# Optimization experiments

Hardware: AMD Instinct MI355X
Metric: run time of the kernel (lower is better)

## Reference

```python
import jax, jax.numpy as jnp
import numpy as np

B = 8388608
NUM_CLASSES = 3
ALPHA = 0.25
GAMMA = 2.0
CRIT_PENALTY = 50.0
PENALTY = np.array([[0.0, 2.0, 5.0], [8.0, 0.0, 3.0], [50.0, 20.0, 0.0]], dtype=np.float32)


def setup_inputs() -> dict:
    key = jax.random.key(0)
    k1, k2 = jax.random.split(key)
    outputs = jax.random.normal(k1, (B, NUM_CLASSES), dtype=jnp.float32)
    targets = jax.random.randint(k2, (B,), 0, NUM_CLASSES, dtype=jnp.int64)
    class_weights = jnp.array([1.0, 2.0, 5.0], dtype=jnp.float32)
    penalty_matrix = jnp.asarray(PENALTY)
    return {"outputs": outputs, "targets": targets,
            "class_weights": class_weights, "penalty_matrix": penalty_matrix}


def reference(outputs, targets, class_weights, penalty_matrix):
    # log-softmax once; per-sample CE
    log_p = jax.nn.log_softmax(outputs, axis=1)                     # [B, C]
    ce_raw = -jnp.take_along_axis(log_p, targets[:, None], axis=1)[:, 0]  # [B]

    # weighted CE with mean reduction (torch: sum(w_t * ce) / sum(w_t))
    w_t = class_weights[targets]                                    # [B]
    ce_loss = jnp.sum(w_t * ce_raw) / jnp.sum(w_t)

    # focal component
    pt = jnp.exp(-ce_raw)
    focal_loss = jnp.mean(ALPHA * (1.0 - pt) ** GAMMA * ce_raw)

    # safety penalty: vectorized gather penalty_matrix[true, pred]
    pred_classes = jnp.argmax(outputs, axis=1)                      # [B]
    safety_penalty = jnp.mean(penalty_matrix[targets, pred_classes])

    # critical-miss penalty (class 2)
    critical_mask = targets == 2
    n_crit = jnp.sum(critical_mask)
    misses = jnp.sum(critical_mask & (pred_classes != 2)).astype(jnp.float32)
    critical_penalty = jnp.where(
        n_crit > 0,
        misses / jnp.maximum(n_crit, 1).astype(jnp.float32) * CRIT_PENALTY,
        0.0,
    )

    total = ce_loss + 0.3 * focal_loss + 0.4 * safety_penalty + 0.6 * critical_penalty
    return total
```

## Files before the change

### kernel.cpp

```cpp
#include <hip/hip_runtime.h>


#define THREADS 256
#define SAMPLES 8
#define SPB (THREADS * SAMPLES)

__global__ __launch_bounds__(THREADS) void loss_main(
    const float* __restrict__ outp,
    const int*   __restrict__ tgt,
    const float* __restrict__ cw,
    const float* __restrict__ pen,
    float*       __restrict__ partial,
    int n, int nblocks)
{
    __shared__ float4 lut[9];
    const int tid = threadIdx.x;
    if (tid < 9) {
        int t = (tid >= 6) ? 2 : ((tid >= 3) ? 1 : 0);
        int p = tid - t * 3;
        float4 e;
        e.x = pen[tid];
        e.y = cw[t];
        e.z = (t == 1) ? 4096.f : ((t == 2) ? 1.f : 0.f);
        e.w = (t == 2 && p != 2) ? 1.f : 0.f;
        lut[tid] = e;
    }
    __syncthreads();

    float s_wce = 0.f, s_f = 0.f, s_s = 0.f, s_cnt = 0.f, s_miss = 0.f;

    const long long base = ((long long)blockIdx.x * THREADS + tid) * SAMPLES;

    if (base + SAMPLES - 1 < n) {
        const float4* o4 = (const float4*)(outp + base * 3);
        const int4*   t4 = (const int4*)(tgt + base);
        float xf[3 * SAMPLES];
        *(float4*)&xf[ 0] = o4[0]; *(float4*)&xf[ 4] = o4[1]; *(float4*)&xf[ 8] = o4[2];
        *(float4*)&xf[12] = o4[3]; *(float4*)&xf[16] = o4[4]; *(float4*)&xf[20] = o4[5];
        int ti[SAMPLES];
        *(int4*)&ti[0] = t4[0]; *(int4*)&ti[4] = t4[1];

#pragma unroll
        for (int k = 0; k < SAMPLES; ++k) {
            float x0 = xf[3*k+0], x1 = xf[3*k+1], x2 = xf[3*k+2];
            int t = ti[k];
            float e0 = __expf(x0);
            float e1 = __expf(x1);
            float e2 = __expf(x2);
            float s  = e0 + e1 + e2;
            bool  t0 = (t == 0), t1 = (t == 1);
            float xt = t0 ? x0 : (t1 ? x1 : x2);
            float et = t0 ? e0 : (t1 ? e1 : e2);
            float ce = __logf(s) - xt;
            float pt = __fdividef(et, s);
            bool  g10 = (x1 > x0);
            int   pred = g10 ? 1 : 0;
            float xp   = g10 ? x1 : x0;
            if (x2 > xp) pred = 2;

            float4 L = lut[t * 3 + pred];
            s_s   += L.x;
            s_wce += L.y * ce;
            float om = 1.f - pt;
            s_f   += om * om * ce;
            s_cnt += L.z;
            s_miss+= L.w;
        }
    } else {
        for (int k = 0; k < SAMPLES; ++k) {
            long long i = base + k;
            if (i >= n) break;
            float x0 = outp[i*3+0], x1 = outp[i*3+1], x2 = outp[i*3+2];
            int t = tgt[i];
            float e0 = __expf(x0), e1 = __expf(x1), e2 = __expf(x2);
            float s  = e0 + e1 + e2;
            bool  t0 = (t == 0), t1 = (t == 1);
            float xt = t0 ? x0 : (t1 ? x1 : x2);
            float et = t0 ? e0 : (t1 ? e1 : e2);
            float ce = __logf(s) - xt;
            float pt = __fdividef(et, s);
            bool  g10 = (x1 > x0);
            int   pred = g10 ? 1 : 0;
            float xp   = g10 ? x1 : x0;
            if (x2 > xp) pred = 2;
            float4 L = lut[t * 3 + pred];
            s_s   += L.x;
            s_wce += L.y * ce;
            float om = 1.f - pt;
            s_f   += om * om * ce;
            s_cnt += L.z;
            s_miss+= L.w;
        }
    }

#pragma unroll
    for (int off = 32; off > 0; off >>= 1) {
        s_wce  += __shfl_down(s_wce,  off);
        s_f    += __shfl_down(s_f,    off);
        s_s    += __shfl_down(s_s,    off);
        s_cnt  += __shfl_down(s_cnt,  off);
        s_miss += __shfl_down(s_miss, off);
    }

    __shared__ float fred[4][5];
    const int lane = tid & 63;
    const int wave = tid >> 6;
    if (lane == 0) {
        fred[wave][0] = s_wce; fred[wave][1] = s_f;  fred[wave][2] = s_s;
        fred[wave][3] = s_cnt; fred[wave][4] = s_miss;
    }
    __syncthreads();
    if (tid < 5) {
        float v = fred[0][tid] + fred[1][tid] + fred[2][tid] + fred[3][tid];
        partial[tid * nblocks + blockIdx.x] = v;
    }
}

__global__ __launch_bounds__(256) void loss_finalize(
    const float* __restrict__ partial,
    float* __restrict__ out, int nblocks, int n)
{
    double a_wce = 0, a_f = 0, a_s = 0, a_n1 = 0, a_n2 = 0, a_miss = 0;
    for (int i = threadIdx.x; i < nblocks; i += 256) {
        a_wce += (double)partial[0 * nblocks + i];
        a_f   += (double)partial[1 * nblocks + i];
        a_s   += (double)partial[2 * nblocks + i];
        float c  = partial[3 * nblocks + i];
        float n1 = floorf(c * (1.f / 4096.f));
        a_n1 += (double)n1;
        a_n2 += (double)(c - n1 * 4096.f);
        a_miss += (double)partial[4 * nblocks + i];
    }
    double acc[6] = {a_wce, a_f, a_s, a_n1, a_n2, a_miss};
#pragma unroll
    for (int off = 32; off > 0; off >>= 1) {
#pragma unroll
        for (int j = 0; j < 6; ++j)
            acc[j] += __shfl_down(acc[j], off);
    }
    __shared__ double dred[4][6];
    const int lane = threadIdx.x & 63;
    const int wave = threadIdx.x >> 6;
    if (lane == 0) {
#pragma unroll
        for (int j = 0; j < 6; ++j) dred[wave][j] = acc[j];
    }
    __syncthreads();
    if (threadIdx.x == 0) {
        double t[6];
#pragma unroll
        for (int j = 0; j < 6; ++j)
            t[j] = dred[0][j] + dred[1][j] + dred[2][j] + dred[3][j];
        double n1 = t[3], n2 = t[4];
        double s_w = (double)n + n1 + 4.0 * n2;
        double inv_b   = 1.0 / (double)n;
        double ce_loss = t[0] / s_w;
        double focal   = 0.25 * t[1] * inv_b;
        double safety  = t[2] * inv_b;
        double crit    = (n2 > 0.0) ? (t[5] / n2 * 50.0) : 0.0;
        out[0] = (float)(ce_loss + 0.3 * focal + 0.4 * safety + 0.6 * crit);
    }
}

extern "C" void kernel_launch(void* const* d_in, const int* in_sizes, int n_in,
                              void* d_out, int out_size, void* d_ws, size_t ws_size,
                              hipStream_t stream) {
    const float* outp = (const float*)d_in[0];
    const int*   tgt  = (const int*)d_in[1];
    const float* cw   = (const float*)d_in[2];
    const float* pen  = (const float*)d_in[3];
    float* out = (float*)d_out;
    const int n = in_sizes[1];

    const int nblocks = (n + SPB - 1) / SPB;
    float* partial = (float*)d_ws;

    loss_main<<<nblocks, THREADS, 0, stream>>>(outp, tgt, cw, pen, partial, n, nblocks);
    loss_finalize<<<1, 256, 0, stream>>>(partial, out, nblocks, n);
}
```

Measured before the change: 179.9 us.

## Switch to persistent grid-stride blocks with register double-buffered tile loads

Replaces the one-tile-per-block launch (4096 blocks) with a fixed grid of 1024 persistent blocks that loop over tiles of 4 samples per thread, prefetching the next tile into registers while the current one is computed. The packed class-1/class-2 count encoding is split into two separate accumulators, which simplifies the finalize step, and the finalize now reduces a fixed 1024 partials. This aims to hide memory latency and cut block launch and reduction overhead for a bandwidth-bound kernel. In exchange each thread issues smaller loads per iteration and the loop adds control overhead, and occupancy depends on 1024 blocks being enough to fill the GPU.

Result: slower. 184.2 us (+2.4%).

```diff
diff --git a/kernel.cpp b/kernel.cpp
--- a/kernel.cpp
+++ b/kernel.cpp
@@ -2,8 +2,23 @@
 
 
 #define THREADS 256
-#define SAMPLES 8
+#define SAMPLES 4
 #define SPB (THREADS * SAMPLES)
+#define NB 1024
+
+typedef float f32x4 __attribute__((ext_vector_type(4)));
+typedef int   i32x4 __attribute__((ext_vector_type(4)));
+
+struct TileRegs {
+    f32x4 o0, o1, o2;
+    i32x4 t0;
+};
+
+__device__ __forceinline__ void load_tile(TileRegs& r, const float* op, const int* tp) {
+    const f32x4* o4 = (const f32x4*)op;
+    r.o0 = o4[0]; r.o1 = o4[1]; r.o2 = o4[2];
+    r.t0 = *(const i32x4*)tp;
+}
 
 __global__ __launch_bounds__(THREADS) void loss_main(
     const float* __restrict__ outp,
@@ -11,7 +26,7 @@
     const float* __restrict__ cw,
     const float* __restrict__ pen,
     float*       __restrict__ partial,
-    int n, int nblocks)
+    int n)
 {
     __shared__ float4 lut[9];
     const int tid = threadIdx.x;
@@ -21,75 +36,85 @@
         float4 e;
         e.x = pen[tid];
         e.y = cw[t];
-        e.z = (t == 1) ? 4096.f : ((t == 2) ? 1.f : 0.f);
+        e.z = (t == 1) ? 1.f : 0.f;
         e.w = (t == 2 && p != 2) ? 1.f : 0.f;
         lut[tid] = e;
     }
     __syncthreads();
 
-    float s_wce = 0.f, s_f = 0.f, s_s = 0.f, s_cnt = 0.f, s_miss = 0.f;
+    float s_wce = 0.f, s_f = 0.f, s_s = 0.f, s_n1 = 0.f, s_n2 = 0.f, s_miss = 0.f;
 
-    const long long base = ((long long)blockIdx.x * THREADS + tid) * SAMPLES;
+    const long long nfull = (long long)n / SPB;
+    long long tl = blockIdx.x;
 
-    if (base + SAMPLES - 1 < n) {
-        const float4* o4 = (const float4*)(outp + base * 3);
-        const int4*   t4 = (const int4*)(tgt + base);
-        float xf[3 * SAMPLES];
-        *(float4*)&xf[ 0] = o4[0]; *(float4*)&xf[ 4] = o4[1]; *(float4*)&xf[ 8] = o4[2];
-        *(float4*)&xf[12] = o4[3]; *(float4*)&xf[16] = o4[4]; *(float4*)&xf[20] = o4[5];
-        int ti[SAMPLES];
-        *(int4*)&ti[0] = t4[0]; *(int4*)&ti[4] = t4[1];
+#define SAMPLE_BODY(x0, x1, x2, t)                                          \
+    {                                                                       \
+        float e0 = __expf(x0);                                              \
+        float e1 = __expf(x1);                                              \
+        float e2 = __expf(x2);                                              \
+        float s  = e0 + e1 + e2;                                            \
+        bool  t0 = ((t) == 0), t1 = ((t) == 1);                             \
+        float xt = t0 ? (x0) : (t1 ? (x1) : (x2));                          \
+        float et = t0 ? e0 : (t1 ? e1 : e2);                                \
+        float ce = __logf(s) - xt;                   \
+        float pt = __fdividef(et, s);                       \
+        bool  g10 = ((x1) > (x0));                                          \
+        int   pred = g10 ? 1 : 0;                                           \
+        float xp   = g10 ? (x1) : (x0);                                     \
+        if ((x2) > xp) pred = 2;                                            \
+        float4 L = lut[(t) * 3 + pred];                                     \
+        s_s   += L.x;                                                       \
+        s_wce += L.y * ce;                                                  \
+        float om = 1.f - pt;                                                \
+        s_f   += om * om * ce;                 \
+        s_n1  += L.z;                                                       \
+        s_n2  += ((t) == 2) ? 1.f : 0.f;                                    \
+        s_miss+= L.w;                                                       \
+    }
 
-#pragma unroll
+#define COMPUTE_TILE(R)                                                     \
+    {                                                                       \
+        float xf[12];                                                       \
+        *(f32x4*)&xf[0] = (R).o0; *(f32x4*)&xf[4] = (R).o1;                 \
+        *(f32x4*)&xf[8] = (R).o2;                                           \
+        int ti[4];                                                          \
+        *(i32x4*)&ti[0] = (R).t0;                                           \
+        _Pragma("unroll")                                                   \
+        for (int k = 0; k < 4; ++k)                                         \
+            SAMPLE_BODY(xf[3*k+0], xf[3*k+1], xf[3*k+2], ti[k]);            \
+    }
+
+    if (tl < nfull) {
+        const long long sbase = tl * SPB + (long long)tid * SAMPLES;
+        const float* op = outp + sbase * 3;
+        const int*   tp = tgt + sbase;
+        const long long stepS = (long long)NB * SPB;
+
+        TileRegs cur, nxt;
+        load_tile(cur, op, tp);
+
+        while (true) {
+            long long tn = tl + NB;
+            bool have_next = (tn < nfull);
+            if (have_next) {
+                op += stepS * 3;
+                tp += stepS;
+                load_tile(nxt, op, tp);
+            }
+            COMPUTE_TILE(cur);
+            if (!have_next) break;
+            cur = nxt;
+            tl = tn;
+        }
+    }
+
+    if ((n % SPB) != 0 && blockIdx.x == (int)(nfull % NB)) {
         for (int k = 0; k < SAMPLES; ++k) {
-            float x0 = xf[3*k+0], x1 = xf[3*k+1], x2 = xf[3*k+2];
-            int t = ti[k];
-            float e0 = __expf(x0);
-            float e1 = __expf(x1);
-            float e2 = __expf(x2);
-            float s  = e0 + e1 + e2;
-            bool  t0 = (t == 0), t1 = (t == 1);
-            float xt = t0 ? x0 : (t1 ? x1 : x2);
-            float et = t0 ? e0 : (t1 ? e1 : e2);
-            float ce = __logf(s) - xt;
-            float pt = __fdividef(et, s);
-            bool  g10 = (x1 > x0);
-            int   pred = g10 ? 1 : 0;
-            float xp   = g10 ? x1 : x0;
-            if (x2 > xp) pred = 2;
-
-            float4 L = lut[t * 3 + pred];
-            s_s   += L.x;
-            s_wce += L.y * ce;
-            float om = 1.f - pt;
-            s_f   += om * om * ce;
-            s_cnt += L.z;
-            s_miss+= L.w;
-        }
-    } else {
-        for (int k = 0; k < SAMPLES; ++k) {
-            long long i = base + k;
+            long long i = nfull * SPB + (long long)tid * SAMPLES + k;
             if (i >= n) break;
             float x0 = outp[i*3+0], x1 = outp[i*3+1], x2 = outp[i*3+2];
             int t = tgt[i];
-            float e0 = __expf(x0), e1 = __expf(x1), e2 = __expf(x2);
-            float s  = e0 + e1 + e2;
-            bool  t0 = (t == 0), t1 = (t == 1);
-            float xt = t0 ? x0 : (t1 ? x1 : x2);
-            float et = t0 ? e0 : (t1 ? e1 : e2);
-            float ce = __logf(s) - xt;
-            float pt = __fdividef(et, s);
-            bool  g10 = (x1 > x0);
-            int   pred = g10 ? 1 : 0;
-            float xp   = g10 ? x1 : x0;
-            if (x2 > xp) pred = 2;
-            float4 L = lut[t * 3 + pred];
-            s_s   += L.x;
-            s_wce += L.y * ce;
-            float om = 1.f - pt;
-            s_f   += om * om * ce;
-            s_cnt += L.z;
-            s_miss+= L.w;
+            SAMPLE_BODY(x0, x1, x2, t);
         }
     }
 
@@ -98,40 +123,35 @@
         s_wce  += __shfl_down(s_wce,  off);
         s_f    += __shfl_down(s_f,    off);
         s_s    += __shfl_down(s_s,    off);
-        s_cnt  += __shfl_down(s_cnt,  off);
+        s_n1   += __shfl_down(s_n1,   off);
+        s_n2   += __shfl_down(s_n2,   off);
         s_miss += __shfl_down(s_miss, off);
     }
 
-    __shared__ float fred[4][5];
+    __shared__ float fred[4][6];
     const int lane = tid & 63;
     const int wave = tid >> 6;
     if (lane == 0) {
-        fred[wave][0] = s_wce; fred[wave][1] = s_f;  fred[wave][2] = s_s;
-        fred[wave][3] = s_cnt; fred[wave][4] = s_miss;
+        fred[wave][0] = s_wce; fred[wave][1] = s_f;    fred[wave][2] = s_s;
+        fred[wave][3] = s_n1;  fred[wave][4] = s_n2;   fred[wave][5] = s_miss;
     }
     __syncthreads();
-    if (tid < 5) {
+    if (tid < 6) {
         float v = fred[0][tid] + fred[1][tid] + fred[2][tid] + fred[3][tid];
-        partial[tid * nblocks + blockIdx.x] = v;
+        partial[tid * NB + blockIdx.x] = v;
     }
 }
 
 __global__ __launch_bounds__(256) void loss_finalize(
     const float* __restrict__ partial,
-    float* __restrict__ out, int nblocks, int n)
+    float* __restrict__ out, int n)
 {
-    double a_wce = 0, a_f = 0, a_s = 0, a_n1 = 0, a_n2 = 0, a_miss = 0;
-    for (int i = threadIdx.x; i < nblocks; i += 256) {
-        a_wce += (double)partial[0 * nblocks + i];
-        a_f   += (double)partial[1 * nblocks + i];
-        a_s   += (double)partial[2 * nblocks + i];
-        float c  = partial[3 * nblocks + i];
-        float n1 = floorf(c * (1.f / 4096.f));
-        a_n1 += (double)n1;
-        a_n2 += (double)(c - n1 * 4096.f);
-        a_miss += (double)partial[4 * nblocks + i];
+    double acc[6] = {0, 0, 0, 0, 0, 0};
+    for (int i = threadIdx.x; i < NB; i += 256) {
+#pragma unroll
+        for (int j = 0; j < 6; ++j)
+            acc[j] += (double)partial[j * NB + i];
     }
-    double acc[6] = {a_wce, a_f, a_s, a_n1, a_n2, a_miss};
 #pragma unroll
     for (int off = 32; off > 0; off >>= 1) {
 #pragma unroll
@@ -172,9 +192,8 @@
     float* out = (float*)d_out;
     const int n = in_sizes[1];
 
-    const int nblocks = (n + SPB - 1) / SPB;
     float* partial = (float*)d_ws;
 
-    loss_main<<<nblocks, THREADS, 0, stream>>>(outp, tgt, cw, pen, partial, n, nblocks);
-    loss_finalize<<<1, 256, 0, stream>>>(partial, out, nblocks, n);
+    loss_main<<<NB, THREADS, 0, stream>>>(outp, tgt, cw, pen, partial, n);
+    loss_finalize<<<1, 256, 0, stream>>>(partial, out, n);
 }
```
